# Kernel tuning notes

Hardware: AMD Instinct MI355X
Metric: run time of the kernel (lower is better)

The kernel has to match this reference:

```python
import math
import jax, jax.numpy as jnp
import numpy as np

N, S, E, H = 8, 1024, 768, 12  # batch, seq_len, n_embed, n_head


def setup_inputs() -> dict:
    key = jax.random.key(0)
    ks = jax.random.split(key, 10)
    s = 1.0 / math.sqrt(E)
    x = jax.random.normal(ks[0], (N, S, E), dtype=jnp.float32)
    # per-head full-width projections, stacked over heads: [H, E, E] (Linear weight layout [out, in])
    Wq = jax.random.normal(ks[1], (H, E, E), dtype=jnp.float32) * s
    Wk = jax.random.normal(ks[2], (H, E, E), dtype=jnp.float32) * s
    Wv = jax.random.normal(ks[3], (H, E, E), dtype=jnp.float32) * s
    bq = jax.random.normal(ks[4], (H, E), dtype=jnp.float32) * s
    bk = jax.random.normal(ks[5], (H, E), dtype=jnp.float32) * s
    bv = jax.random.normal(ks[6], (H, E), dtype=jnp.float32) * s
    Wc = jax.random.normal(ks[7], (E, H * E), dtype=jnp.float32) * (1.0 / math.sqrt(H * E))
    bc = jax.random.normal(ks[8], (E,), dtype=jnp.float32) * s
    return {"x": x, "Wq": Wq, "bq": bq, "Wk": Wk, "bk": bk, "Wv": Wv, "bv": bv, "Wc": Wc, "bc": bc}


def reference(x, Wq, bq, Wk, bk, Wv, bv, Wc, bc):
    # Full-width QKV per head: [H, N, S, E]
    q = jnp.einsum('nse,hde->hnsd', x, Wq) + bq[:, None, None, :]
    k = jnp.einsum('nse,hde->hnsd', x, Wk) + bk[:, None, None, :]
    v = jnp.einsum('nse,hde->hnsd', x, Wv) + bv[:, None, None, :]
    # scores scaled by sqrt(n_embed) (source quirk: full n_embed, not head_dim)
    scores = jnp.einsum('hnsd,hntd->hnst', q, k) / math.sqrt(E)
    causal = jnp.tril(jnp.ones((S, S), dtype=bool))
    scores = jnp.where(causal[None, None, :, :], scores, -jnp.inf)
    # dropout applied before softmax in source; p=0 (eval) -> identity
    attn = jax.nn.softmax(scores, axis=-1)
    heads = jnp.einsum('hnst,hntd->hnsd', attn, v)  # [H, N, S, E]
    concat = jnp.transpose(heads, (1, 2, 0, 3)).reshape(N, S, H * E)
    return concat @ Wc.T + bc
```

## Files before the change

kernel.cpp:

```cpp
#include <hip/hip_runtime.h>
#include <hip/hip_bf16.h>
#include <stdint.h>

#define SEQ    1024
#define NBAT   8
#define EMB    768
#define NHEAD  12
#define MROWS  (NBAT*SEQ)
#define SCALE_S 0.03608439182435161f

typedef unsigned short u16;
typedef __attribute__((ext_vector_type(8))) short bf16x8;
typedef __attribute__((ext_vector_type(4))) float f32x4;

typedef void __attribute__((address_space(1)))* gas_ptr;
typedef void __attribute__((address_space(3)))* las_ptr;

__device__ __forceinline__ void gload16(const void* g, void* l) {
  __builtin_amdgcn_global_load_lds((gas_ptr)(void*)g, (las_ptr)l, 16, 0, 0);
}

#define VMCNT0 asm volatile("s_waitcnt vmcnt(0)" ::: "memory")
#define VMCNT2 asm volatile("s_waitcnt vmcnt(2)" ::: "memory")
#define VMCNT4 asm volatile("s_waitcnt vmcnt(4)" ::: "memory")
#define VMCNT6 asm volatile("s_waitcnt vmcnt(6)" ::: "memory")
#define LGKM0  asm volatile("s_waitcnt lgkmcnt(0)" ::: "memory")
#define BARRIER asm volatile("s_barrier" ::: "memory")

__device__ __forceinline__ u16 f2bf(float f) {
  union { float f; uint32_t u; } a; a.f = f;
  uint32_t r = a.u + 0x7fffu + ((a.u >> 16) & 1u);
  return (u16)(r >> 16);
}
__device__ __forceinline__ float bf2f(u16 b) {
  union { uint32_t u; float f; } c; c.u = (uint32_t)b << 16; return c.f;
}
__device__ __forceinline__ uint32_t pack2(float a, float b) {
  return (uint32_t)f2bf(a) | ((uint32_t)f2bf(b) << 16);
}

__global__ void k_cvt(const float* __restrict__ s, u16* __restrict__ d, long n) {
  long i = ((long)blockIdx.x*blockDim.x + threadIdx.x)*8;
  if (i >= n) return;
  float4 a = *(const float4*)(s+i);
  float4 b = *(const float4*)(s+i+4);
  uint4 o; o.x = pack2(a.x,a.y); o.y = pack2(a.z,a.w);
  o.z = pack2(b.x,b.y); o.w = pack2(b.z,b.w);
  *(uint4*)(d+i) = o;
}

__global__ void k_cvtT(const float* __restrict__ wq, const float* __restrict__ wk,
                       u16* __restrict__ dq, u16* __restrict__ dk, int Gi) {
  __shared__ float t[64][65];
  int z = blockIdx.z;
  const float* src = (z < Gi) ? wq + (size_t)z*EMB*EMB : wk + (size_t)(z-Gi)*EMB*EMB;
  u16* dst = (z < Gi) ? dq + (size_t)z*EMB*EMB : dk + (size_t)(z-Gi)*EMB*EMB;
  int d0 = blockIdx.x*64, e0 = blockIdx.y*64;
  int tt = threadIdx.x;
  int el = tt & 63, db = tt >> 6;
  #pragma unroll
  for (int p = 0; p < 16; ++p) {
    int dl = p*4 + db;
    t[dl][el] = src[(size_t)(d0+dl)*EMB + e0 + el];
  }
  __syncthreads();
  int dl2 = tt & 63, eb = tt >> 6;
  #pragma unroll
  for (int p = 0; p < 16; ++p) {
    int e2 = p*4 + eb;
    dst[(size_t)(e0+e2)*EMB + d0 + dl2] = f2bf(t[dl2][e2]);
  }
}

__global__ void k_cvtwc(const float* __restrict__ wc, u16* __restrict__ d, int Gi, int h0) {
  long ncol = (long)Gi*EMB;
  long i = ((long)blockIdx.x*blockDim.x + threadIdx.x)*4;
  if (i >= 768*ncol) return;
  long eo = i / ncol, c = i - eo*ncol;
  long g = c / EMB, dd = c - g*EMB;
  const float* s = wc + eo*(long)(NHEAD*EMB) + (h0+g)*EMB + dd;
  float4 a = *(const float4*)s;
  uint2 o; o.x = pack2(a.x,a.y); o.y = pack2(a.z,a.w);
  *(uint2*)(d+i) = o;
}

__global__ void k_mka(const u16* __restrict__ wkT, const float* __restrict__ bq,
                      float* __restrict__ a) {
  int g = blockIdx.y;
  int e = blockIdx.x*256 + threadIdx.x;
  const u16* row = wkT + (size_t)g*EMB*EMB + (size_t)e*EMB;
  const float* b = bq + (size_t)g*EMB;
  float s = 0.f;
  for (int d = 0; d < EMB; ++d) s += bf2f(row[d]) * b[d];
  a[(size_t)g*EMB + e] = s;
}

__global__ void k_mkv(const u16* __restrict__ xb, const float* __restrict__ a,
                      float* __restrict__ v) {
  int g = blockIdx.y;
  int w = threadIdx.x >> 6, l = threadIdx.x & 63;
  int i = blockIdx.x*8 + w;
  const u16* xr = xb + (size_t)i*EMB;
  const float* ag = a + (size_t)g*EMB;
  float s = 0.f;
  #pragma unroll
  for (int c = 0; c < 12; ++c) {
    int e = c*64 + l;
    s += bf2f(xr[e]) * ag[e];
  }
  s += __shfl_xor(s, 1); s += __shfl_xor(s, 2); s += __shfl_xor(s, 4);
  s += __shfl_xor(s, 8); s += __shfl_xor(s, 16); s += __shfl_xor(s, 32);
  if (l == 0) v[(size_t)g*MROWS + i] = s;
}

struct Gemm256Args {
  const u16* A; int lda;
  const u16* B; int ldb; int K;
  u16* Cb; long c_hs; int ldc;
  const float* bias; const float* bias2;
  int gsplit; int mode; int swap;
};

__global__ __launch_bounds__(512, 2) void k_gemm256d(Gemm256Args p0, Gemm256Args p1)
{
  __shared__ u16 lsA[2*16384];
  __shared__ u16 lsB[2*16384];

  const Gemm256Args P = blockIdx.z ? p1 : p0;
  int m0 = (P.swap ? blockIdx.y : blockIdx.x) * 256;
  int n0 = (P.swap ? blockIdx.x : blockIdx.y) * 256;
  int tid = threadIdx.x;
  int w = tid >> 6, l = tid & 63;
  int wr = w >> 2, wc = w & 3;

  const u16* gA = P.A + (size_t)(m0 + 32*w + (l>>3))*P.lda + (((l&7) ^ (l>>3)) << 3);
  const u16* gB = P.B + (size_t)(n0 + 32*w + (l>>3))*P.ldb + (((l&7) ^ (l>>3)) << 3);

#define STAGE256(t, buf) do { \
    int k0_ = (t)*64; \
    _Pragma("unroll") \
    for (int c_ = 0; c_ < 4; ++c_) \
      gload16(gA + (size_t)(c_*8)*P.lda + k0_, lsA + (buf)*16384 + (32*w + 8*c_)*64); \
    _Pragma("unroll") \
    for (int c_ = 0; c_ < 4; ++c_) \
      gload16(gB + (size_t)(c_*8)*P.ldb + k0_, lsB + (buf)*16384 + (32*w + 8*c_)*64); \
  } while(0)

  f32x4 acc[8][4];
  #pragma unroll
  for (int i = 0; i < 8; ++i)
    #pragma unroll
    for (int j = 0; j < 4; ++j) acc[i][j] = (f32x4)0.0f;

  int nt = P.K >> 6;
  STAGE256(0, 0);
  for (int t = 0; t < nt; ++t) {
    VMCNT0; BARRIER;
    if (t + 1 < nt) STAGE256(t+1, (t+1)&1);
    const u16* la = lsA + (t&1)*16384;
    const u16* lb = lsB + (t&1)*16384;
    #pragma unroll
    for (int ks = 0; ks < 2; ++ks) {
      int off = (((4*ks + (l>>4)) ^ (l&7)) << 3);
      bf16x8 af[8], bf_[4];
      #pragma unroll
      for (int fi = 0; fi < 8; ++fi)
        af[fi] = *(const bf16x8*)(la + (wr*128 + fi*16 + (l&15))*64 + off);
      #pragma unroll
      for (int fj = 0; fj < 4; ++fj)
        bf_[fj] = *(const bf16x8*)(lb + (wc*64 + fj*16 + (l&15))*64 + off);
      __builtin_amdgcn_s_setprio(1);
      #pragma unroll
      for (int fi = 0; fi < 8; ++fi)
        #pragma unroll
        for (int fj = 0; fj < 4; ++fj)
          acc[fi][fj] = __builtin_amdgcn_mfma_f32_16x16x32_bf16(af[fi], bf_[fj], acc[fi][fj], 0, 0, 0);
      __builtin_amdgcn_s_setprio(0);
    }
  }
#undef STAGE256

  if (P.mode == 0) {
    int s = n0 / 768;
    int dbase = n0 - s*768 + wc*64;
    const float* bsl = P.bias ? ((s < P.gsplit) ? P.bias + (size_t)s*768
                                                : P.bias2 + (size_t)(s - P.gsplit)*768)
                              : (const float*)0;
    u16* Cs = P.Cb + (size_t)s*P.c_hs;
    #pragma unroll
    for (int fj = 0; fj < 4; ++fj) {
      int dcol = dbase + fj*16 + (l&15);
      float bb = bsl ? bsl[dcol] : 0.f;
      #pragma unroll
      for (int fi = 0; fi < 8; ++fi) {
        #pragma unroll
        for (int r = 0; r < 4; ++r) {
          int row = m0 + wr*128 + fi*16 + (l>>4)*4 + r;
          Cs[(size_t)row*768 + dcol] = f2bf(acc[fi][fj][r] + bb);
        }
      }
    }
  } else {
    #pragma unroll
    for (int fi = 0; fi < 8; ++fi) {
      #pragma unroll
      for (int r = 0; r < 4; ++r) {
        int row = m0 + wr*128 + fi*16 + (l>>4)*4 + r;
        float bb = P.bias[row];
        #pragma unroll
        for (int fj = 0; fj < 4; ++fj) {
          int cbn = n0 + wc*64 + fj*16 + (l&15);
          P.Cb[(size_t)row*P.ldc + cbn] = f2bf(acc[fi][fj][r] + bb);
        }
      }
    }
  }
}

__global__ __launch_bounds__(256) void k_gemm(
    const u16* __restrict__ A, long a_hs, int lda,
    const u16* __restrict__ B, long b_hs, int ldb, int K,
    u16* Cb, float* Cf, long c_hs, int ldc,
    const float* __restrict__ bias, const float* __restrict__ bias2,
    long bias_hs, int gsplit, int mode, int swapxy)
{
  __shared__ u16 lsA[3*4096];
  __shared__ u16 lsB[3*4096];
  int g = blockIdx.z;
  const u16* Ag = A + (long)g*a_hs;
  const u16* Bg = B + (long)g*b_hs;
  int tm = swapxy ? blockIdx.y : blockIdx.x;
  int tn = swapxy ? blockIdx.x : blockIdx.y;
  int m0 = tm*128, n0 = tn*128;
  int tid = threadIdx.x;
  int w = tid >> 6, l = tid & 63;

  int srow = l >> 2;
  int scol = ((l & 3) ^ ((l >> 3) & 3)) * 8;
  const u16* ga0 = Ag + (long)(m0 + (2*w)*16   + srow)*lda + scol;
  const u16* ga1 = Ag + (long)(m0 + (2*w+1)*16 + srow)*lda + scol;
  const u16* gb0 = Bg + (long)(n0 + (2*w)*16   + srow)*ldb + scol;
  const u16* gb1 = Bg + (long)(n0 + (2*w+1)*16 + srow)*ldb + scol;

#define GSTAGE(k0, buf) do { \
    gload16(ga0 + (k0), lsA + (buf)*4096 + (2*w)*512); \
    gload16(ga1 + (k0), lsA + (buf)*4096 + (2*w+1)*512); \
    gload16(gb0 + (k0), lsB + (buf)*4096 + (2*w)*512); \
    gload16(gb1 + (k0), lsB + (buf)*4096 + (2*w+1)*512); \
  } while(0)

  f32x4 acc[4][4];
  #pragma unroll
  for (int i = 0; i < 4; ++i)
    #pragma unroll
    for (int j = 0; j < 4; ++j) acc[i][j] = (f32x4)0.0f;

  int wr = w >> 1, wc_ = w & 1;
  int frow = l & 15;
  int sp = (l >> 4) ^ ((frow >> 1) & 3);
  int aoff[4], boff[4];
  #pragma unroll
  for (int i = 0; i < 4; ++i) {
    aoff[i] = (wr*64 + i*16 + frow)*32 + sp*8;
    boff[i] = (wc_*64 + i*16 + frow)*32 + sp*8;
  }

  int nt = K >> 5;
  GSTAGE(0, 0);
  GSTAGE(32, 1);
  VMCNT4; BARRIER;
  int cur = 0;
  for (int t = 0; t < nt; ++t) {
    if (t + 2 < nt) {
      int nb = cur + 2; if (nb >= 3) nb -= 3;
      GSTAGE((t+2) << 5, nb);
    }
    const u16* la = lsA + cur*4096;
    const u16* lb = lsB + cur*4096;
    bf16x8 af[4], bfr[4];
    #pragma unroll
    for (int i = 0; i < 4; ++i) af[i] = *(const bf16x8*)(la + aoff[i]);
    #pragma unroll
    for (int j = 0; j < 4; ++j) bfr[j] = *(const bf16x8*)(lb + boff[j]);
    #pragma unroll
    for (int i = 0; i < 4; ++i)
      #pragma unroll
      for (int j = 0; j < 4; ++j)
        acc[i][j] = __builtin_amdgcn_mfma_f32_16x16x32_bf16(af[i], bfr[j], acc[i][j], 0, 0, 0);
    if (t + 2 < nt) { VMCNT4; } else { VMCNT0; }
    LGKM0; BARRIER;
    cur = (cur == 2) ? 0 : cur + 1;
  }
#undef GSTAGE

  u16* Cbg = Cb ? Cb + (long)g*c_hs : (u16*)0;
  const float* bsel = (g < gsplit) ? bias : bias2;
  long gi = (g < gsplit) ? g : g - gsplit;
  const float* bs = bsel ? bsel + gi*bias_hs : (const float*)0;
  int rl = (l >> 4)*4, cl = l & 15;
  #pragma unroll
  for (int i = 0; i < 4; ++i) {
    #pragma unroll
    for (int j = 0; j < 4; ++j) {
      int rb = m0 + wr*64 + i*16 + rl;
      int cb = n0 + wc_*64 + j*16 + cl;
      float cbv = 0.f;
      if ((mode == 0 || mode == 2) && bs) cbv = bs[cb];
      #pragma unroll
      for (int r = 0; r < 4; ++r) {
        int rr = rb + r;
        float v = acc[i][j][r];
        v += (mode == 1) ? bs[rr] : cbv;
        size_t idx = (size_t)rr*(size_t)ldc + cb;
        if (mode <= 1) Cbg[idx] = f2bf(v);
        else if (mode == 2) Cf[idx] = v;
        else Cf[idx] += v;
      }
    }
  }
}

__global__ __launch_bounds__(256, 2) void k_attn(
    const u16* __restrict__ qb, const u16* __restrict__ xkb,
    const u16* __restrict__ vtb, const float* __restrict__ vh,
    u16* __restrict__ hb, int ldh)
{
  __shared__ u16 kls[2*8192];
  __shared__ u16 vls[2*8192];
  __shared__ float s_t[32*68];
  __shared__ u16 p_t[32*64];
  __shared__ float e_s[32];

  int b = blockIdx.x;
  int xcd = b & 7, kk_ = b >> 3;
  int pair = kk_ & 15;
  int gn = xcd + 8*(kk_ >> 4);
  int g = gn >> 3, n = gn & 7;

  const u16* Q  = qb  + (size_t)g*MROWS*EMB + (size_t)n*SEQ*EMB;
  const u16* Kp = xkb + (size_t)n*SEQ*EMB;
  const u16* Vt = vtb + (size_t)g*EMB*MROWS + (size_t)n*SEQ;
  const float* Vh = vh + (size_t)g*MROWS + (size_t)n*SEQ;
  u16* H = hb + (size_t)(n*SEQ)*ldh + (size_t)g*EMB;

  int tid = threadIdx.x;
  int w = tid >> 6, l = tid & 63;
  int qg = w >> 1;
  int cg = w & 1;
  int frow = l & 15;
  int fsw = frow & 7;
  int hi = l >> 4;
  int srow = tid >> 3;
  int sphys = tid & 7;
  int scol = ((sphys ^ (srow & 7)) << 3);

#define KSTAGE(base, pc, buf) do { \
    const u16* s_ = (base) + (size_t)srow*EMB + (pc)*128 + scol; \
    u16* d_ = kls + (buf)*8192 + w*512; \
    gload16(s_,                  d_); \
    gload16(s_ + (size_t)32*EMB, d_ + 2048); \
    gload16(s_ + 64,                  d_ + 4096); \
    gload16(s_ + (size_t)32*EMB + 64, d_ + 6144); \
  } while(0)
#define VSTAGE(vc, buf) do { \
    const u16* s_ = Vt + (size_t)((vc)*128 + srow)*MROWS + t0 + scol; \
    u16* d_ = vls + (buf)*8192 + w*512; \
    gload16(s_,                       d_); \
    gload16(s_ + (size_t)32*MROWS,    d_ + 2048); \
    gload16(s_ + (size_t)64*MROWS,    d_ + 4096); \
    gload16(s_ + (size_t)96*MROWS,    d_ + 6144); \
  } while(0)
#define QSTAGE(pc, dst) do { \
    const u16* s_ = Q + (size_t)(q0 + srow)*EMB + (pc)*128 + scol; \
    gload16(s_,      (dst) + w*512); \
    gload16(s_ + 64, (dst) + 2048 + w*512); \
  } while(0)
#define RD_Q(pc, src) do { \
    _Pragma("unroll") for (int kk2 = 0; kk2 < 2; ++kk2) \
      _Pragma("unroll") for (int kkl = 0; kkl < 2; ++kkl) \
        qreg[2*(pc) + kk2][kkl] = *(const bf16x8*)((src) + kk2*2048 + (qg*16 + frow)*64 \
                                                   + (((kkl*4 + hi) ^ fsw) << 3)); \
  } while(0)
#define QK_PH(c, buf) do { \
    const u16* kb_ = kls + (buf)*8192; \
    __builtin_amdgcn_s_setprio(1); \
    _Pragma("unroll") for (int kk2 = 0; kk2 < 2; ++kk2) \
      _Pragma("unroll") for (int kkl = 0; kkl < 2; ++kkl) { \
        int so = ((kkl*4 + hi) ^ fsw) << 3; \
        bf16x8 aq = qreg[2*(c) + kk2][kkl]; \
        _Pragma("unroll") for (int cc = 0; cc < 2; ++cc) { \
          bf16x8 bk_ = *(const bf16x8*)(kb_ + kk2*4096 + ((cg*2 + cc)*16 + frow)*64 + so); \
          sacc[cc] = __builtin_amdgcn_mfma_f32_16x16x32_bf16(aq, bk_, sacc[cc], 0, 0, 0); \
        } \
      } \
    __builtin_amdgcn_s_setprio(0); \
  } while(0)
#define PV_PH(c, buf) do { \
    const u16* vb_ = vls + (buf)*8192; \
    __builtin_amdgcn_s_setprio(1); \
    _Pragma("unroll") for (int cf = 0; cf < 4; ++cf) \
      _Pragma("unroll") for (int kk = 0; kk < 2; ++kk) { \
        bf16x8 vbf = *(const bf16x8*)(vb_ + (cg*64 + cf*16 + frow)*64 + (((kk*4 + hi) ^ fsw) << 3)); \
        acc[(c)][cf] = __builtin_amdgcn_mfma_f32_16x16x32_bf16(pa[kk], vbf, acc[(c)][cf], 0, 0, 0); \
      } \
    __builtin_amdgcn_s_setprio(0); \
  } while(0)

  for (int half = 0; half < 2; ++half) {
    int qt = half ? 31 - pair : pair;
    int q0 = qt * 32;
    int ntk = (qt >> 1) + 1;
    int qglob = q0 + srow;

    f32x4 acc[6][4];
    #pragma unroll
    for (int i = 0; i < 6; ++i)
      #pragma unroll
      for (int j = 0; j < 4; ++j) acc[i][j] = (f32x4)0.0f;
    float m_reg = -1e30f, l_reg = 0.f;

    bf16x8 qreg[12][2];
    VMCNT0;
    QSTAGE(0, kls); QSTAGE(1, kls + 8192); QSTAGE(2, vls); QSTAGE(3, vls + 8192);
    VMCNT6; BARRIER;
    RD_Q(0, kls);          VMCNT4; LGKM0; BARRIER;
    QSTAGE(4, kls);        RD_Q(1, kls + 8192); VMCNT4; LGKM0; BARRIER;
    QSTAGE(5, kls + 8192); RD_Q(2, vls);        VMCNT4; LGKM0; BARRIER;
    RD_Q(3, vls + 8192);   VMCNT2; LGKM0; BARRIER;
    RD_Q(4, kls);          VMCNT0; LGKM0; BARRIER;
    KSTAGE(Kp, 0, 0);      RD_Q(5, kls + 8192); VMCNT0; LGKM0; BARRIER;

    for (int tt = 0; tt < ntk; ++tt) {
      int t0 = tt*64;
      const u16* Kb  = Kp + (size_t)t0*EMB;
      const u16* Kbn = Kp + (size_t)(t0 + 64)*EMB;
      bool sn = (tt + 1 < ntk);
      float vv0 = Vh[t0 + cg*32 + frow];
      float vv1 = Vh[t0 + cg*32 + 16 + frow];

      f32x4 sacc[2]; sacc[0] = (f32x4)0.0f; sacc[1] = (f32x4)0.0f;
      KSTAGE(Kb, 1, 1);  QK_PH(0, 0);  VMCNT0; BARRIER;
      KSTAGE(Kb, 2, 0);  QK_PH(1, 1);  VMCNT0; BARRIER;
      KSTAGE(Kb, 3, 1);  QK_PH(2, 0);  VMCNT0; BARRIER;
      KSTAGE(Kb, 4, 0);  QK_PH(3, 1);  VMCNT0; BARRIER;
      KSTAGE(Kb, 5, 1);  QK_PH(4, 0);  VMCNT0; BARRIER;
      VSTAGE(0, 0);      QK_PH(5, 1);
      #pragma unroll
      for (int r = 0; r < 4; ++r) {
        s_t[(qg*16 + hi*4 + r)*68 + cg*32 + frow]      = (sacc[0][r] + vv0)*SCALE_S;
        s_t[(qg*16 + hi*4 + r)*68 + cg*32 + 16 + frow] = (sacc[1][r] + vv1)*SCALE_S;
      }
      VMCNT0; LGKM0; BARRIER;
      VSTAGE(1, 1);
      {
        int cbase = t0 + sphys*8;
        float v[8]; float mx = -1e30f;
        #pragma unroll
        for (int j = 0; j < 8; ++j) {
          float s = s_t[srow*68 + sphys*8 + j];
          if (cbase + j > qglob) s = -1e30f;
          v[j] = s; mx = fmaxf(mx, s);
        }
        mx = fmaxf(mx, __shfl_xor(mx, 1));
        mx = fmaxf(mx, __shfl_xor(mx, 2));
        mx = fmaxf(mx, __shfl_xor(mx, 4));
        float mn = fmaxf(m_reg, mx);
        float esc = __expf(m_reg - mn);
        float ps = 0.f; u16 pk[8];
        #pragma unroll
        for (int j = 0; j < 8; ++j) { float p = __expf(v[j] - mn); ps += p; pk[j] = f2bf(p); }
        ps += __shfl_xor(ps, 1); ps += __shfl_xor(ps, 2); ps += __shfl_xor(ps, 4);
        l_reg = l_reg*esc + ps; m_reg = mn;
        if (sphys == 0) e_s[srow] = esc;
        uint4 pv;
        pv.x = (uint32_t)pk[0] | ((uint32_t)pk[1] << 16);
        pv.y = (uint32_t)pk[2] | ((uint32_t)pk[3] << 16);
        pv.z = (uint32_t)pk[4] | ((uint32_t)pk[5] << 16);
        pv.w = (uint32_t)pk[6] | ((uint32_t)pk[7] << 16);
        *(uint4*)(p_t + srow*64 + ((sphys ^ (srow & 7)) << 3)) = pv;
      }
      LGKM0; BARRIER;
      float er[4];
      #pragma unroll
      for (int r = 0; r < 4; ++r) er[r] = e_s[qg*16 + hi*4 + r];
      #pragma unroll
      for (int i = 0; i < 6; ++i)
        #pragma unroll
        for (int j = 0; j < 4; ++j)
          #pragma unroll
          for (int r = 0; r < 4; ++r) acc[i][j][r] *= er[r];
      bf16x8 pa[2];
      #pragma unroll
      for (int kk = 0; kk < 2; ++kk)
        pa[kk] = *(const bf16x8*)(p_t + (qg*16 + frow)*64 + (((kk*4 + hi) ^ fsw) << 3));
      PV_PH(0, 0);       VMCNT0; BARRIER;
      VSTAGE(2, 0);      PV_PH(1, 1);  VMCNT0; BARRIER;
      VSTAGE(3, 1);      PV_PH(2, 0);  VMCNT0; BARRIER;
      VSTAGE(4, 0);      PV_PH(3, 1);  VMCNT0; BARRIER;
      VSTAGE(5, 1);      PV_PH(4, 0);  VMCNT0; BARRIER;
      if (sn) KSTAGE(Kbn, 0, 0);
      PV_PH(5, 1);       VMCNT0; BARRIER;
    }

    if (sphys == 0) e_s[srow] = l_reg;
    LGKM0; BARRIER;
    float linv[4];
    #pragma unroll
    for (int r = 0; r < 4; ++r) linv[r] = 1.0f / e_s[qg*16 + hi*4 + r];
    #pragma unroll
    for (int i = 0; i < 6; ++i)
      #pragma unroll
      for (int j = 0; j < 4; ++j) {
        int col = i*128 + cg*64 + j*16 + (l & 15);
        #pragma unroll
        for (int r = 0; r < 4; ++r) {
          int row = q0 + qg*16 + hi*4 + r;
          H[(size_t)row*ldh + col] = f2bf(acc[i][j][r]*linv[r]);
        }
      }
    BARRIER;
  }
#undef KSTAGE
#undef VSTAGE
#undef QSTAGE
#undef RD_Q
#undef QK_PH
#undef PV_PH
}

extern "C" void kernel_launch(void* const* d_in, const int* in_sizes, int n_in,
                              void* d_out, int out_size, void* d_ws, size_t ws_size,
                              hipStream_t stream) {
  const float* x  = (const float*)d_in[0];
  const float* Wq = (const float*)d_in[1];
  const float* bq = (const float*)d_in[2];
  const float* Wk = (const float*)d_in[3];
  const float* bv = (const float*)d_in[6];
  const float* Wv = (const float*)d_in[5];
  const float* Wc = (const float*)d_in[7];
  const float* bc = (const float*)d_in[8];
  float* out = (float*)d_out;

  const size_t XB  = (size_t)MROWS*EMB*sizeof(u16);
  const size_t WHB = (size_t)EMB*EMB*sizeof(u16);
  const size_t VHB = (size_t)MROWS*sizeof(float);
  const size_t AB  = (size_t)EMB*sizeof(float);
  const size_t fixed = XB + 36*WHB + 12*(VHB + AB) + 8192;
  int G = 4;
  while (G > 2 && fixed + (size_t)G*3*XB > ws_size) --G;

  char* ws = (char*)d_ws;
  u16* xb  = (u16*)ws;  ws += XB;
  u16* wvb = (u16*)ws;  ws += 12*WHB;
  u16* wcb = (u16*)ws;  ws += 12*WHB;
  u16* mtb = (u16*)ws;  ws += 12*WHB;
  float* vh = (float*)ws; ws += 12*VHB;
  float* ab = (float*)ws; ws += 12*AB;
  u16* yb  = (u16*)ws;  ws += (size_t)G*XB;
  u16* vtb = (u16*)ws;  ws += (size_t)G*XB;
  u16* hbf = (u16*)ws;  ws += (size_t)G*XB;
  u16* wqT = hbf;
  u16* wkT = vtb;

  k_cvt<<<dim3(3072), dim3(256), 0, stream>>>(x, xb, (long)MROWS*EMB);
  k_cvtT<<<dim3(12, 12, 24), dim3(256), 0, stream>>>(Wq, Wk, wqT, wkT, 12);
  k_cvt<<<dim3((unsigned)((12L*EMB*EMB/8)/256)), dim3(256), 0, stream>>>(
      Wv, wvb, 12L*EMB*EMB);
  k_cvtwc<<<dim3((unsigned)((768L*12*EMB/4)/256)), dim3(256), 0, stream>>>(Wc, wcb, 12, 0);
  k_gemm<<<dim3(6, 6, 12), dim3(256), 0, stream>>>(
      wkT, (long)EMB*EMB, EMB, wqT, (long)EMB*EMB, EMB, EMB,
      mtb, (float*)0, (long)EMB*EMB, EMB,
      (const float*)0, (const float*)0, 0L, 9999, 0, 0);
  k_mka<<<dim3(3, 12), dim3(256), 0, stream>>>(wkT, bq, ab);
  k_mkv<<<dim3(1024, 12), dim3(512), 0, stream>>>(xb, ab, vh);

  for (int h0 = 0; h0 < NHEAD; h0 += G) {
    int Gi = (G < NHEAD - h0) ? G : (NHEAD - h0);
    Gemm256Args ay = { xb, EMB, mtb + (size_t)h0*EMB*EMB, EMB, EMB,
                       yb, (long)MROWS*EMB, 768,
                       (const float*)0, (const float*)0, Gi, 0, 0 };
    Gemm256Args av = { wvb + (size_t)h0*EMB*EMB, EMB, xb, EMB, EMB,
                       vtb, 0L, MROWS,
                       bv + (size_t)h0*EMB, (const float*)0, 9999, 1, 1 };
    k_gemm256d<<<dim3(32, 3*Gi, 2), dim3(512), 0, stream>>>(ay, av);
    k_attn<<<dim3(16*NBAT*Gi), dim3(256), 0, stream>>>(
        yb, xb, vtb, vh + (size_t)h0*MROWS, hbf, Gi*EMB);
    k_gemm<<<dim3(64, 6, 1), dim3(256), 0, stream>>>(
        hbf, 0L, Gi*EMB, wcb + (size_t)h0*EMB, 0L, NHEAD*EMB, Gi*EMB,
        (u16*)0, out, 0L, EMB,
        (h0 == 0 ? bc : (const float*)0), (const float*)0, 0L, 9999,
        (h0 == 0 ? 2 : 3), 0);
  }
}
```

Baseline: 1.139 ms.

## Enlarge attention tiles to 64 query rows with 512 threads and deeper staging

```diff
diff --git a/kernel.cpp b/kernel.cpp
--- a/kernel.cpp
+++ b/kernel.cpp
@@ -320,21 +320,20 @@
   }
 }
 
-__global__ __launch_bounds__(256, 2) void k_attn(
+__global__ __launch_bounds__(512, 2) void k_attn(
     const u16* __restrict__ qb, const u16* __restrict__ xkb,
     const u16* __restrict__ vtb, const float* __restrict__ vh,
     u16* __restrict__ hb, int ldh)
 {
-  __shared__ u16 kls[2*8192];
-  __shared__ u16 vls[2*8192];
-  __shared__ float s_t[32*68];
-  __shared__ u16 p_t[32*64];
-  __shared__ float e_s[32];
+  __shared__ u16 kls[4*8192];
+  __shared__ u16 vls[4*8192];
+  __shared__ float s_t[64*68];
+  __shared__ u16 p_t[64*64];
+  __shared__ float e_s[64];
 
   int b = blockIdx.x;
   int xcd = b & 7, kk_ = b >> 3;
-  int pair = kk_ & 15;
-  int gn = xcd + 8*(kk_ >> 4);
+  int gn = xcd + 8*(kk_ >> 3), pair = kk_ & 7;
   int g = gn >> 3, n = gn & 7;
 
   const u16* Q  = qb  + (size_t)g*MROWS*EMB + (size_t)n*SEQ*EMB;
@@ -349,68 +348,64 @@
   int cg = w & 1;
   int frow = l & 15;
   int fsw = frow & 7;
-  int hi = l >> 4;
   int srow = tid >> 3;
   int sphys = tid & 7;
   int scol = ((sphys ^ (srow & 7)) << 3);
 
-#define KSTAGE(base, pc, buf) do { \
-    const u16* s_ = (base) + (size_t)srow*EMB + (pc)*128 + scol; \
-    u16* d_ = kls + (buf)*8192 + w*512; \
-    gload16(s_,                  d_); \
-    gload16(s_ + (size_t)32*EMB, d_ + 2048); \
-    gload16(s_ + 64,                  d_ + 4096); \
-    gload16(s_ + (size_t)32*EMB + 64, d_ + 6144); \
-  } while(0)
-#define VSTAGE(vc, buf) do { \
-    const u16* s_ = Vt + (size_t)((vc)*128 + srow)*MROWS + t0 + scol; \
-    u16* d_ = vls + (buf)*8192 + w*512; \
-    gload16(s_,                       d_); \
-    gload16(s_ + (size_t)32*MROWS,    d_ + 2048); \
-    gload16(s_ + (size_t)64*MROWS,    d_ + 4096); \
-    gload16(s_ + (size_t)96*MROWS,    d_ + 6144); \
-  } while(0)
-#define QSTAGE(pc, dst) do { \
-    const u16* s_ = Q + (size_t)(q0 + srow)*EMB + (pc)*128 + scol; \
-    gload16(s_,      (dst) + w*512); \
-    gload16(s_ + 64, (dst) + 2048 + w*512); \
-  } while(0)
-#define RD_Q(pc, src) do { \
+#define KSTG(base, pc) do { \
+    const u16* s_ = (base) + (pc)*128; \
+    u16* d_ = kls + ((pc)&3)*8192 + w*512; \
+    gload16(s_,      d_); \
+    gload16(s_ + 64, d_ + 4096); \
+  } while(0)
+#define VSTG(vc) do { \
+    const u16* s_ = Vs + (size_t)((vc)*128)*MROWS; \
+    u16* d_ = vls + ((vc)&3)*8192 + w*512; \
+    gload16(s_,                    d_); \
+    gload16(s_ + (size_t)64*MROWS, d_ + 4096); \
+  } while(0)
+#define QSTG(pc, arr) do { \
+    const u16* s_ = Qs + (pc)*128; \
+    gload16(s_,      (arr) + w*512); \
+    gload16(s_ + 64, (arr) + 4096 + w*512); \
+  } while(0)
+#define RD_Q(pc, arr) do { \
     _Pragma("unroll") for (int kk2 = 0; kk2 < 2; ++kk2) \
       _Pragma("unroll") for (int kkl = 0; kkl < 2; ++kkl) \
-        qreg[2*(pc) + kk2][kkl] = *(const bf16x8*)((src) + kk2*2048 + (qg*16 + frow)*64 \
-                                                   + (((kkl*4 + hi) ^ fsw) << 3)); \
-  } while(0)
-#define QK_PH(c, buf) do { \
-    const u16* kb_ = kls + (buf)*8192; \
+        qreg[2*(pc) + kk2][kkl] = *(const bf16x8*)((arr) + kk2*4096 + (qg*16 + frow)*64 \
+                                                   + (((kkl*4 + (l>>4)) ^ fsw) << 3)); \
+  } while(0)
+#define QK_PH(c) do { \
+    const u16* kb_ = kls + ((c)&3)*8192; \
     __builtin_amdgcn_s_setprio(1); \
-    _Pragma("unroll") for (int kk2 = 0; kk2 < 2; ++kk2) \
+    _Pragma("unroll") for (int kk2 = 0; kk2 < 2; ++kk2) { \
       _Pragma("unroll") for (int kkl = 0; kkl < 2; ++kkl) { \
-        int so = ((kkl*4 + hi) ^ fsw) << 3; \
+        int so = ((kkl*4 + (l>>4)) ^ fsw) << 3; \
         bf16x8 aq = qreg[2*(c) + kk2][kkl]; \
         _Pragma("unroll") for (int cc = 0; cc < 2; ++cc) { \
           bf16x8 bk_ = *(const bf16x8*)(kb_ + kk2*4096 + ((cg*2 + cc)*16 + frow)*64 + so); \
           sacc[cc] = __builtin_amdgcn_mfma_f32_16x16x32_bf16(aq, bk_, sacc[cc], 0, 0, 0); \
         } \
       } \
+    } \
     __builtin_amdgcn_s_setprio(0); \
   } while(0)
-#define PV_PH(c, buf) do { \
-    const u16* vb_ = vls + (buf)*8192; \
+#define PV_PH(c) do { \
+    const u16* vb_ = vls + ((c)&3)*8192; \
     __builtin_amdgcn_s_setprio(1); \
-    _Pragma("unroll") for (int cf = 0; cf < 4; ++cf) \
+    _Pragma("unroll") for (int cf = 0; cf < 4; ++cf) { \
       _Pragma("unroll") for (int kk = 0; kk < 2; ++kk) { \
-        bf16x8 vbf = *(const bf16x8*)(vb_ + (cg*64 + cf*16 + frow)*64 + (((kk*4 + hi) ^ fsw) << 3)); \
+        bf16x8 vbf = *(const bf16x8*)(vb_ + (cg*64 + cf*16 + frow)*64 + (((kk*4 + (l>>4)) ^ fsw) << 3)); \
         acc[(c)][cf] = __builtin_amdgcn_mfma_f32_16x16x32_bf16(pa[kk], vbf, acc[(c)][cf], 0, 0, 0); \
       } \
+    } \
     __builtin_amdgcn_s_setprio(0); \
   } while(0)
 
   for (int half = 0; half < 2; ++half) {
-    int qt = half ? 31 - pair : pair;
-    int q0 = qt * 32;
-    int ntk = (qt >> 1) + 1;
-    int qglob = q0 + srow;
+    int qt = half ? 15 - pair : pair;
+    int q0 = qt * 64;
+    int nt = qt + 1;
 
     f32x4 acc[6][4];
     #pragma unroll
@@ -419,40 +414,45 @@
       for (int j = 0; j < 4; ++j) acc[i][j] = (f32x4)0.0f;
     float m_reg = -1e30f, l_reg = 0.f;
 
+    const u16* Qs  = Q + (size_t)(q0 + srow)*EMB + scol;
+    const u16* Ks0 = Kp + (size_t)srow*EMB + scol;
     bf16x8 qreg[12][2];
     VMCNT0;
-    QSTAGE(0, kls); QSTAGE(1, kls + 8192); QSTAGE(2, vls); QSTAGE(3, vls + 8192);
+    QSTG(0, kls); QSTG(1, kls + 8192); QSTG(2, kls + 16384); QSTG(3, kls + 24576);
     VMCNT6; BARRIER;
-    RD_Q(0, kls);          VMCNT4; LGKM0; BARRIER;
-    QSTAGE(4, kls);        RD_Q(1, kls + 8192); VMCNT4; LGKM0; BARRIER;
-    QSTAGE(5, kls + 8192); RD_Q(2, vls);        VMCNT4; LGKM0; BARRIER;
-    RD_Q(3, vls + 8192);   VMCNT2; LGKM0; BARRIER;
-    RD_Q(4, kls);          VMCNT0; LGKM0; BARRIER;
-    KSTAGE(Kp, 0, 0);      RD_Q(5, kls + 8192); VMCNT0; LGKM0; BARRIER;
-
-    for (int tt = 0; tt < ntk; ++tt) {
+    QSTG(4, vls);       RD_Q(0, kls);         VMCNT6; LGKM0; BARRIER;
+    QSTG(5, vls + 8192); RD_Q(1, kls + 8192); VMCNT6; LGKM0; BARRIER;
+    KSTG(Ks0, 0);       RD_Q(2, kls + 16384); VMCNT6; LGKM0; BARRIER;
+    KSTG(Ks0, 1);       RD_Q(3, kls + 24576); VMCNT6; LGKM0; BARRIER;
+    KSTG(Ks0, 2);       RD_Q(4, vls);         VMCNT6; LGKM0; BARRIER;
+                        RD_Q(5, vls + 8192);  LGKM0;
+
+    for (int tt = 0; tt < nt; ++tt) {
       int t0 = tt*64;
-      const u16* Kb  = Kp + (size_t)t0*EMB;
-      const u16* Kbn = Kp + (size_t)(t0 + 64)*EMB;
-      bool sn = (tt + 1 < ntk);
+      const u16* Ks  = Kp + (size_t)(t0 + srow)*EMB + scol;
+      const u16* Ksn = Kp + (size_t)(t0 + 64 + srow)*EMB + scol;
+      const u16* Vs  = Vt + (size_t)srow*MROWS + t0 + scol;
+      bool sn = (tt + 1 < nt);
       float vv0 = Vh[t0 + cg*32 + frow];
       float vv1 = Vh[t0 + cg*32 + 16 + frow];
+      VMCNT4; BARRIER;
 
       f32x4 sacc[2]; sacc[0] = (f32x4)0.0f; sacc[1] = (f32x4)0.0f;
-      KSTAGE(Kb, 1, 1);  QK_PH(0, 0);  VMCNT0; BARRIER;
-      KSTAGE(Kb, 2, 0);  QK_PH(1, 1);  VMCNT0; BARRIER;
-      KSTAGE(Kb, 3, 1);  QK_PH(2, 0);  VMCNT0; BARRIER;
-      KSTAGE(Kb, 4, 0);  QK_PH(3, 1);  VMCNT0; BARRIER;
-      KSTAGE(Kb, 5, 1);  QK_PH(4, 0);  VMCNT0; BARRIER;
-      VSTAGE(0, 0);      QK_PH(5, 1);
+      KSTG(Ks, 3); QK_PH(0); VMCNT4; LGKM0; BARRIER;
+      KSTG(Ks, 4); QK_PH(1); VMCNT4; LGKM0; BARRIER;
+      KSTG(Ks, 5); QK_PH(2); VMCNT4; LGKM0; BARRIER;
+      VSTG(0);     QK_PH(3); VMCNT4; LGKM0; BARRIER;
+      VSTG(1);     QK_PH(4); VMCNT4; LGKM0; BARRIER;
+      VSTG(2);     QK_PH(5);
       #pragma unroll
       for (int r = 0; r < 4; ++r) {
-        s_t[(qg*16 + hi*4 + r)*68 + cg*32 + frow]      = (sacc[0][r] + vv0)*SCALE_S;
-        s_t[(qg*16 + hi*4 + r)*68 + cg*32 + 16 + frow] = (sacc[1][r] + vv1)*SCALE_S;
+        s_t[(qg*16 + (l>>4)*4 + r)*68 + cg*32 + frow]      = (sacc[0][r] + vv0)*SCALE_S;
+        s_t[(qg*16 + (l>>4)*4 + r)*68 + cg*32 + 16 + frow] = (sacc[1][r] + vv1)*SCALE_S;
       }
-      VMCNT0; LGKM0; BARRIER;
-      VSTAGE(1, 1);
+      LGKM0; BARRIER;
+      VSTG(3);
       {
+        int qglob = q0 + srow;
         int cbase = t0 + sphys*8;
         float v[8]; float mx = -1e30f;
         #pragma unroll
@@ -479,10 +479,10 @@
         pv.w = (uint32_t)pk[6] | ((uint32_t)pk[7] << 16);
         *(uint4*)(p_t + srow*64 + ((sphys ^ (srow & 7)) << 3)) = pv;
       }
-      LGKM0; BARRIER;
+      VMCNT6; LGKM0; BARRIER;
       float er[4];
       #pragma unroll
-      for (int r = 0; r < 4; ++r) er[r] = e_s[qg*16 + hi*4 + r];
+      for (int r = 0; r < 4; ++r) er[r] = e_s[qg*16 + (l>>4)*4 + r];
       #pragma unroll
       for (int i = 0; i < 6; ++i)
         #pragma unroll
@@ -492,21 +492,28 @@
       bf16x8 pa[2];
       #pragma unroll
       for (int kk = 0; kk < 2; ++kk)
-        pa[kk] = *(const bf16x8*)(p_t + (qg*16 + frow)*64 + (((kk*4 + hi) ^ fsw) << 3));
-      PV_PH(0, 0);       VMCNT0; BARRIER;
-      VSTAGE(2, 0);      PV_PH(1, 1);  VMCNT0; BARRIER;
-      VSTAGE(3, 1);      PV_PH(2, 0);  VMCNT0; BARRIER;
-      VSTAGE(4, 0);      PV_PH(3, 1);  VMCNT0; BARRIER;
-      VSTAGE(5, 1);      PV_PH(4, 0);  VMCNT0; BARRIER;
-      if (sn) KSTAGE(Kbn, 0, 0);
-      PV_PH(5, 1);       VMCNT0; BARRIER;
+        pa[kk] = *(const bf16x8*)(p_t + (qg*16 + frow)*64 + (((kk*4 + (l>>4)) ^ fsw) << 3));
+                   PV_PH(0); VMCNT4; LGKM0; BARRIER;
+      VSTG(4);     PV_PH(1); VMCNT4; LGKM0; BARRIER;
+      VSTG(5);     PV_PH(2); VMCNT4; LGKM0; BARRIER;
+      if (sn) KSTG(Ksn, 0);
+                   PV_PH(3);
+      if (sn) { VMCNT4; } else { VMCNT2; }
+      LGKM0; BARRIER;
+      if (sn) KSTG(Ksn, 1);
+                   PV_PH(4);
+      if (sn) { VMCNT4; } else { VMCNT0; }
+      LGKM0; BARRIER;
+      if (sn) KSTG(Ksn, 2);
+                   PV_PH(5);
+      if (!sn) { VMCNT0; LGKM0; BARRIER; }
     }
 
     if (sphys == 0) e_s[srow] = l_reg;
     LGKM0; BARRIER;
     float linv[4];
     #pragma unroll
-    for (int r = 0; r < 4; ++r) linv[r] = 1.0f / e_s[qg*16 + hi*4 + r];
+    for (int r = 0; r < 4; ++r) linv[r] = 1.0f / e_s[qg*16 + (l>>4)*4 + r];
     #pragma unroll
     for (int i = 0; i < 6; ++i)
       #pragma unroll
@@ -514,15 +521,15 @@
         int col = i*128 + cg*64 + j*16 + (l & 15);
         #pragma unroll
         for (int r = 0; r < 4; ++r) {
-          int row = q0 + qg*16 + hi*4 + r;
+          int row = q0 + qg*16 + (l>>4)*4 + r;
           H[(size_t)row*ldh + col] = f2bf(acc[i][j][r]*linv[r]);
         }
       }
     BARRIER;
   }
-#undef KSTAGE
-#undef VSTAGE
-#undef QSTAGE
+#undef KSTG
+#undef VSTG
+#undef QSTG
 #undef RD_Q
 #undef QK_PH
 #undef PV_PH
@@ -583,7 +590,7 @@
                        vtb, 0L, MROWS,
                        bv + (size_t)h0*EMB, (const float*)0, 9999, 1, 1 };
     k_gemm256d<<<dim3(32, 3*Gi, 2), dim3(512), 0, stream>>>(ay, av);
-    k_attn<<<dim3(16*NBAT*Gi), dim3(256), 0, stream>>>(
+    k_attn<<<dim3(8*NBAT*Gi), dim3(512), 0, stream>>>(
         yb, xb, vtb, vh + (size_t)h0*MROWS, hbf, Gi*EMB);
     k_gemm<<<dim3(64, 6, 1), dim3(256), 0, stream>>>(
         hbf, 0L, Gi*EMB, wcb + (size_t)h0*EMB, 0L, NHEAD*EMB, Gi*EMB,
```

Result: faster. 1.069 ms (-6.1%).
